# Optimization experiments

Hardware: AMD Instinct MI355X
Metric: run time of the kernel (lower is better)

Reference implementation:

```python
import jax, jax.numpy as jnp
import numpy as np

N = 100000
E = 3_200_000
H = 64
R = 2
NEG = 0.01   # leaky_relu default slope
EPS = 1e-5   # BatchNorm eps


def leaky(x):
    return jnp.where(x > 0, x, NEG * x)


def bn(x, g, b, m, v):
    # BatchNorm1d in eval mode (running statistics)
    return (x - m) * jax.lax.rsqrt(v + EPS) * g + b


def setup_inputs() -> dict:
    key = jax.random.key(0)
    ks = jax.random.split(key, 16)
    d = {}
    d["des"] = jax.random.normal(ks[0], (N, 768), jnp.float32)
    d["num"] = jax.random.normal(ks[1], (N, 5), jnp.float32)
    d["cat"] = jax.random.normal(ks[2], (N, 6), jnp.float32)
    d["edge_index"] = jax.random.randint(ks[3], (2, E), 0, N)
    d["edge_type"] = jax.random.randint(ks[4], (E,), 0, R)

    def lin(k, o, i):
        return (jax.random.normal(k, (o, i), jnp.float32) / np.float32(np.sqrt(i)))

    # projection heads: Linear + BatchNorm1d params
    d["des_W"] = lin(ks[5], H, 768); d["des_b"] = jnp.zeros((H,), jnp.float32)
    d["num_W"] = lin(ks[6], H, 5);   d["num_b"] = jnp.zeros((H,), jnp.float32)
    d["cat_W"] = lin(ks[7], H, 6);   d["cat_b"] = jnp.zeros((H,), jnp.float32)
    for name, kk in (("des", ks[8]), ("num", ks[9]), ("cat", ks[10])):
        d[name + "_g"] = jnp.ones((H,), jnp.float32)
        d[name + "_beta"] = jnp.zeros((H,), jnp.float32)
        d[name + "_m"] = 0.1 * jax.random.normal(kk, (H,), jnp.float32)
        d[name + "_v"] = jnp.ones((H,), jnp.float32)
    # RGCN relation weights [R, in, out] (used as F.linear(x, W[r]) -> x @ W[r].T)
    d["rgcn_W"] = jax.random.normal(ks[11], (R, H, H), jnp.float32) / np.float32(np.sqrt(H))
    # classifier
    d["cls_W1"] = lin(ks[12], H // 2, H); d["cls_b1"] = jnp.zeros((H // 2,), jnp.float32)
    d["cls_W2"] = lin(ks[13], 2, H // 2); d["cls_b2"] = jnp.zeros((2,), jnp.float32)
    return d


def reference(des, num, cat, edge_index, edge_type,
              des_W, des_b, des_g, des_beta, des_m, des_v,
              num_W, num_b, num_g, num_beta, num_m, num_v,
              cat_W, cat_b, cat_g, cat_beta, cat_m, cat_v,
              rgcn_W, cls_W1, cls_b1, cls_W2, cls_b2):
    # feature fusion: three Linear+BN+LeakyReLU branches summed
    x = leaky(bn(des @ des_W.T + des_b, des_g, des_beta, des_m, des_v))
    x = x + leaky(bn(num @ num_W.T + num_b, num_g, num_beta, num_m, num_v))
    x = x + leaky(bn(cat @ cat_W.T + cat_b, cat_g, cat_beta, cat_m, cat_v))

    # SimpleRGCNConv: per-relation linear transform + masked scatter-mean over edges
    src, dst = edge_index[0], edge_index[1]  # PyG: row=source, col=target
    n = x.shape[0]
    acc = jnp.zeros((n, H), x.dtype)
    for r in range(R):
        x_r = x @ rgcn_W[r].T                       # F.linear(x, weight[r])
        mask = (edge_type == r).astype(x.dtype)     # [E]
        msg = x_r[src] * mask[:, None]              # gather + mask
        s = jax.ops.segment_sum(msg, dst, num_segments=n)
        cnt = jax.ops.segment_sum(mask, dst, num_segments=n)
        acc = acc + s / jnp.maximum(cnt, 1.0)[:, None]  # mean; 0 for isolated nodes
    x = leaky(acc / R)  # mean over relations

    # dropout in eval mode is identity; classifier
    h = leaky(x @ cls_W1.T + cls_b1)
    return h @ cls_W2.T + cls_b2
```

## Files before the change

kernel.cpp:

```cpp
#include <hip/hip_runtime.h>

typedef unsigned int u32;
typedef unsigned short u16;

#define NEG 0.01f
#define BN_EPS 1e-5f

typedef __attribute__((ext_vector_type(8))) short bf16x8;
typedef __attribute__((ext_vector_type(4))) float f32x4;

__device__ __forceinline__ float bl(u32 u){ union { u32 i; float f; } c; c.i = u << 16; return c.f; }
__device__ __forceinline__ float bh(u32 u){ union { u32 i; float f; } c; c.i = u & 0xFFFF0000u; return c.f; }
__device__ __forceinline__ u16 f2b(float f){
  union { float f; u32 i; } c; c.f = f;
  u32 t = c.i + 0x7FFFu + ((c.i >> 16) & 1u);
  return (u16)(t >> 16);
}
__device__ __forceinline__ float leaky(float v){ return v > 0.f ? v : NEG * v; }

__global__ __launch_bounds__(256) void k_hist_prep(
    const int* __restrict__ ei, const int* __restrict__ et, int E, int HB, int PB,
    int* __restrict__ deg2,
    const float* __restrict__ desWf, const float* __restrict__ rgcnW,
    const float* __restrict__ W1, u16* __restrict__ tab,
    const float* __restrict__ des, u16* __restrict__ des16, int n)
{
  int bid = blockIdx.x;
  if (bid < HB) {
    int e = bid * 256 + threadIdx.x;
    if (e < E) atomicAdd(&deg2[ei[E + e] * 2 + et[e]], 1);
  } else if (bid < HB + PB) {
    int i = (bid - HB) * 256 + threadIdx.x;
    if (i < 49152) {
      int j = i & 7, lane = (i >> 3) & 63, t = (i >> 9) & 3, k = i >> 11;
      int row = 16 * t + (lane & 15);
      int col = 32 * k + 8 * (lane >> 4) + j;
      tab[i] = f2b(desWf[row * 768 + col]);
    } else if (i < 57344) {
      int j = i - 49152;
      int h = j >> 7, k = j & 127;
      tab[i] = f2b(rgcnW[(k >= 64 ? 4096 : 0) + h * 64 + (k & 63)]);
    } else if (i < 59392) {
      tab[i] = f2b(W1[i - 57344]);
    }
  } else {
    int fb = bid - HB - PB;
    const int tid = threadIdx.x;
    u16* outb = des16 + (size_t)fb * 49152;
    #pragma unroll 4
    for (int it = 0; it < 24; ++it) {
      int s = it * 256 + tid;
      int lane = s & 63;
      int k = (s >> 6) % 24;
      int w = s / 1536;
      int row = fb * 64 + 16 * w + (lane & 15);
      if (row > n - 1) row = n - 1;
      int col = 32 * k + 8 * (lane >> 4);
      const float* p = des + (size_t)row * 768 + col;
      float4 u = *(const float4*)p;
      float4 v = *(const float4*)(p + 4);
      int4 o4;
      o4.x = (int)((u32)f2b(u.x) | ((u32)f2b(u.y) << 16));
      o4.y = (int)((u32)f2b(u.z) | ((u32)f2b(u.w) << 16));
      o4.z = (int)((u32)f2b(v.x) | ((u32)f2b(v.y) << 16));
      o4.w = (int)((u32)f2b(v.z) | ((u32)f2b(v.w) << 16));
      *(int4*)(outb + (size_t)s * 8) = o4;
    }
  }
}

__global__ __launch_bounds__(256) void k_fuse_scan(
    const u16* __restrict__ des16, const float* __restrict__ nump, const float* __restrict__ catp,
    const u16* __restrict__ Wpk, const float* __restrict__ desB,
    const float* __restrict__ numW, const float* __restrict__ numB,
    const float* __restrict__ catW, const float* __restrict__ catB,
    const float* __restrict__ dg, const float* __restrict__ dbe, const float* __restrict__ dm, const float* __restrict__ dv,
    const float* __restrict__ ng, const float* __restrict__ nbe, const float* __restrict__ nm, const float* __restrict__ nv,
    const float* __restrict__ cg, const float* __restrict__ cbe, const float* __restrict__ cm, const float* __restrict__ cv,
    u16* __restrict__ x16, int n,
    const int* __restrict__ deg2, int* __restrict__ offs2, int M)
{
  const int tid  = threadIdx.x;
  const int lane = tid & 63;
  const int w    = tid >> 6;

  if (blockIdx.x == 0) {
    __shared__ int wsum[4];
    __shared__ int carry;
    if (tid == 0) carry = 0;
    __syncthreads();
    for (int base = 0; base < M; base += 1024) {
      int idx = base + tid * 4;
      int4 v = {0, 0, 0, 0};
      if (idx < M) v = *(const int4*)(deg2 + idx);
      int s4 = v.x + v.y + v.z + v.w;
      int s = s4;
      #pragma unroll
      for (int o = 1; o < 64; o <<= 1) { int t = __shfl_up(s, o); if (lane >= o) s += t; }
      if (lane == 63) wsum[w] = s;
      __syncthreads();
      if (tid == 0) {
        int a = wsum[0];
        a += wsum[1]; wsum[1] = a;
        a += wsum[2]; wsum[2] = a;
        a += wsum[3]; wsum[3] = a;
      }
      __syncthreads();
      int wbase = (w == 0) ? 0 : wsum[w - 1];
      int ebase = carry + wbase + (s - s4);
      if (idx < M) {
        int4 o4;
        o4.x = ebase;
        o4.y = ebase + v.x;
        o4.z = ebase + v.x + v.y;
        o4.w = ebase + v.x + v.y + v.z;
        *(int4*)(offs2 + idx) = o4;
      }
      __syncthreads();
      if (tid == 0) carry += wsum[3];
      __syncthreads();
    }
    if (tid == 0) offs2[M] = carry;
    return;
  }

  __shared__ float ync[64][66];

  const int quad = lane >> 4;
  const int l15  = lane & 15;
  const int fb   = blockIdx.x - 1;
  const int rowbase = fb * 64 + 16 * w;

  {
    float nw[5], cw[6];
    #pragma unroll
    for (int j = 0; j < 5; ++j) nw[j] = numW[lane * 5 + j];
    #pragma unroll
    for (int j = 0; j < 6; ++j) cw[j] = catW[lane * 6 + j];
    float An = ng[lane] * rsqrtf(nv[lane] + BN_EPS);
    float Bn = (numB[lane] - nm[lane]) * An + nbe[lane];
    float Ac = cg[lane] * rsqrtf(cv[lane] + BN_EPS);
    float Bc = (catB[lane] - cm[lane]) * Ac + cbe[lane];
    for (int m = 0; m < 16; ++m) {
      int node = rowbase + m; if (node > n - 1) node = n - 1;
      float yn = 0.f, yc = 0.f;
      #pragma unroll
      for (int j = 0; j < 5; ++j) yn = fmaf(nump[node * 5 + j], nw[j], yn);
      #pragma unroll
      for (int j = 0; j < 6; ++j) yc = fmaf(catp[node * 6 + j], cw[j], yc);
      ync[16 * w + m][lane] = leaky(yn * An + Bn) + leaky(yc * Ac + Bc);
    }
  }

  float Ad4[4], Bd4[4];
  #pragma unroll
  for (int t = 0; t < 4; ++t) {
    int nn = 16 * t + l15;
    float A = dg[nn] * rsqrtf(dv[nn] + BN_EPS);
    Ad4[t] = A;
    Bd4[t] = (desB[nn] - dm[nn]) * A + dbe[nn];
  }
  __syncthreads();

  const u16* aP = des16 + (size_t)(fb * 4 + w) * 12288 + lane * 8;
  const u16* bP = Wpk + lane * 8;

  f32x4 acc[4];
  #pragma unroll
  for (int t = 0; t < 4; ++t) acc[t] = (f32x4){0.f, 0.f, 0.f, 0.f};

  #pragma unroll 4
  for (int k = 0; k < 24; ++k) {
    bf16x8 a = *(const bf16x8*)(aP + k * 512);
    acc[0] = __builtin_amdgcn_mfma_f32_16x16x32_bf16(a, *(const bf16x8*)(bP + k * 2048       ), acc[0], 0, 0, 0);
    acc[1] = __builtin_amdgcn_mfma_f32_16x16x32_bf16(a, *(const bf16x8*)(bP + k * 2048 +  512), acc[1], 0, 0, 0);
    acc[2] = __builtin_amdgcn_mfma_f32_16x16x32_bf16(a, *(const bf16x8*)(bP + k * 2048 + 1024), acc[2], 0, 0, 0);
    acc[3] = __builtin_amdgcn_mfma_f32_16x16x32_bf16(a, *(const bf16x8*)(bP + k * 2048 + 1536), acc[3], 0, 0, 0);
  }

  #pragma unroll
  for (int t = 0; t < 4; ++t) {
    #pragma unroll
    for (int r = 0; r < 4; ++r) {
      int m = quad * 4 + r;
      int node = rowbase + m;
      if (node < n) {
        int nn = 16 * t + l15;
        float v = leaky(acc[t][r] * Ad4[t] + Bd4[t]) + ync[16 * w + m][nn];
        x16[(size_t)node * 64 + nn] = f2b(v);
      }
    }
  }
}

__global__ void k_place(const int* __restrict__ ei, const int* __restrict__ et, int E,
                        const int* __restrict__ offs2, int* __restrict__ cur2, int* __restrict__ packed)
{
  int e = blockIdx.x * 256 + threadIdx.x;
  if (e < E) {
    int bin = ei[E + e] * 2 + et[e];
    int pos = offs2[bin] + atomicAdd(&cur2[bin], 1);
    packed[pos] = ei[e];
  }
}

__global__ __launch_bounds__(256) void k_agg(
    const u16* __restrict__ x16, const int* __restrict__ offs2, const int* __restrict__ packed,
    u32* __restrict__ agg, int n)
{
  const int tid = threadIdx.x, lane = tid & 63, w = tid >> 6;
  const int c = lane & 31, half = lane >> 5;

  for (int nd = blockIdx.x * 4 + w; nd < n; nd += gridDim.x * 4) {
    int o0 = offs2[nd * 2], o1 = offs2[nd * 2 + 1], o2 = offs2[nd * 2 + 2];
    float aE[2], aO[2];

    #pragma unroll
    for (int rel = 0; rel < 2; ++rel) {
      int beg = rel ? o1 : o0;
      int end = rel ? o2 : o1;
      float accE = 0.f, accO = 0.f;
      for (int j0 = beg; j0 < end; j0 += 64) {
        int idx = j0 + lane;
        int p = (idx < end) ? packed[idx] : 0;
        p = (p < 0) ? 0 : ((p > n - 1) ? (n - 1) : p);
        int cn = end - j0; if (cn > 64) cn = 64;
        int t = 0;
        for (; t + 16 <= cn; t += 16) {
          int s0 = __shfl(p, t      + half);
          int s1 = __shfl(p, t + 2  + half);
          int s2 = __shfl(p, t + 4  + half);
          int s3 = __shfl(p, t + 6  + half);
          int s4 = __shfl(p, t + 8  + half);
          int s5 = __shfl(p, t + 10 + half);
          int s6 = __shfl(p, t + 12 + half);
          int s7 = __shfl(p, t + 14 + half);
          u32 v0 = *(const u32*)(x16 + (size_t)s0 * 64 + 2 * c);
          u32 v1 = *(const u32*)(x16 + (size_t)s1 * 64 + 2 * c);
          u32 v2 = *(const u32*)(x16 + (size_t)s2 * 64 + 2 * c);
          u32 v3 = *(const u32*)(x16 + (size_t)s3 * 64 + 2 * c);
          u32 v4 = *(const u32*)(x16 + (size_t)s4 * 64 + 2 * c);
          u32 v5 = *(const u32*)(x16 + (size_t)s5 * 64 + 2 * c);
          u32 v6 = *(const u32*)(x16 + (size_t)s6 * 64 + 2 * c);
          u32 v7 = *(const u32*)(x16 + (size_t)s7 * 64 + 2 * c);
          accE += ((bl(v0) + bl(v1)) + (bl(v2) + bl(v3))) + ((bl(v4) + bl(v5)) + (bl(v6) + bl(v7)));
          accO += ((bh(v0) + bh(v1)) + (bh(v2) + bh(v3))) + ((bh(v4) + bh(v5)) + (bh(v6) + bh(v7)));
        }
        for (; t + 8 <= cn; t += 8) {
          int s0 = __shfl(p, t     + half);
          int s1 = __shfl(p, t + 2 + half);
          int s2 = __shfl(p, t + 4 + half);
          int s3 = __shfl(p, t + 6 + half);
          u32 v0 = *(const u32*)(x16 + (size_t)s0 * 64 + 2 * c);
          u32 v1 = *(const u32*)(x16 + (size_t)s1 * 64 + 2 * c);
          u32 v2 = *(const u32*)(x16 + (size_t)s2 * 64 + 2 * c);
          u32 v3 = *(const u32*)(x16 + (size_t)s3 * 64 + 2 * c);
          accE += (bl(v0) + bl(v1)) + (bl(v2) + bl(v3));
          accO += (bh(v0) + bh(v1)) + (bh(v2) + bh(v3));
        }
        for (; t + 2 <= cn; t += 2) {
          int s0 = __shfl(p, t + half);
          u32 v0 = *(const u32*)(x16 + (size_t)s0 * 64 + 2 * c);
          accE += bl(v0); accO += bh(v0);
        }
        if (t < cn) {
          int s0 = __shfl(p, t);
          if (half == 0) {
            u32 v0 = *(const u32*)(x16 + (size_t)s0 * 64 + 2 * c);
            accE += bl(v0); accO += bh(v0);
          }
        }
      }
      accE += __shfl_xor(accE, 32);
      accO += __shfl_xor(accO, 32);
      int cnt = end - beg;
      float sc = 1.f / (float)(cnt > 1 ? cnt : 1);
      aE[rel] = accE * sc;
      aO[rel] = accO * sc;
    }

    float sE = half ? aE[1] : aE[0];
    float sO = half ? aO[1] : aO[0];
    agg[(size_t)nd * 64 + lane] = (u32)f2b(sE) | ((u32)f2b(sO) << 16);
  }
}

__global__ __launch_bounds__(256) void k_mlp(
    const u32* __restrict__ agg, const u16* __restrict__ Wmlp, const u16* __restrict__ W1p,
    const float* __restrict__ b1, const float* __restrict__ W2, const float* __restrict__ b2,
    float2* __restrict__ out, int n)
{
  __shared__ __align__(16) u16 h1[4][16][72];
  __shared__ float h2[4][16][34];

  const int tid = threadIdx.x, lane = tid & 63, w = tid >> 6;
  const int quad = lane >> 4, l15 = lane & 15;
  const int rowbase = blockIdx.x * 64 + 16 * w;

  int rowA = rowbase + l15; if (rowA > n - 1) rowA = n - 1;
  const u16* aRow = (const u16*)(agg + (size_t)rowA * 64);

  f32x4 acc[4];
  #pragma unroll
  for (int t = 0; t < 4; ++t) acc[t] = (f32x4){0.f, 0.f, 0.f, 0.f};
  #pragma unroll
  for (int ks = 0; ks < 4; ++ks) {
    bf16x8 a = *(const bf16x8*)(aRow + ks * 32 + quad * 8);
    #pragma unroll
    for (int t = 0; t < 4; ++t) {
      bf16x8 b = *(const bf16x8*)(Wmlp + (size_t)(16 * t + l15) * 128 + ks * 32 + quad * 8);
      acc[t] = __builtin_amdgcn_mfma_f32_16x16x32_bf16(a, b, acc[t], 0, 0, 0);
    }
  }
  #pragma unroll
  for (int t = 0; t < 4; ++t)
    #pragma unroll
    for (int r = 0; r < 4; ++r) {
      int m = quad * 4 + r;
      h1[w][m][16 * t + l15] = f2b(leaky(0.5f * acc[t][r]));
    }
  __syncthreads();

  f32x4 acc2[2];
  acc2[0] = (f32x4){0.f, 0.f, 0.f, 0.f};
  acc2[1] = (f32x4){0.f, 0.f, 0.f, 0.f};
  #pragma unroll
  for (int ks = 0; ks < 2; ++ks) {
    bf16x8 a = *(const bf16x8*)(&h1[w][l15][ks * 32 + quad * 8]);
    #pragma unroll
    for (int t = 0; t < 2; ++t) {
      bf16x8 b = *(const bf16x8*)(W1p + (size_t)(16 * t + l15) * 64 + ks * 32 + quad * 8);
      acc2[t] = __builtin_amdgcn_mfma_f32_16x16x32_bf16(a, b, acc2[t], 0, 0, 0);
    }
  }
  #pragma unroll
  for (int t = 0; t < 2; ++t)
    #pragma unroll
    for (int r = 0; r < 4; ++r) {
      int m = quad * 4 + r;
      int j = 16 * t + l15;
      h2[w][m][j] = leaky(acc2[t][r] + b1[j]);
    }
  __syncthreads();

  float t0 = 0.f, t1 = 0.f;
  #pragma unroll
  for (int jj = 0; jj < 8; ++jj) {
    int j = quad * 8 + jj;
    float hv = h2[w][l15][j];
    t0 = fmaf(hv, W2[j], t0);
    t1 = fmaf(hv, W2[32 + j], t1);
  }
  t0 += __shfl_xor(t0, 16); t0 += __shfl_xor(t0, 32);
  t1 += __shfl_xor(t1, 16); t1 += __shfl_xor(t1, 32);
  int node = rowbase + l15;
  if (quad == 0 && node < n) {
    float2 q; q.x = t0 + b2[0]; q.y = t1 + b2[1];
    out[node] = q;
  }
}

extern "C" void kernel_launch(void* const* d_in, const int* in_sizes, int n_in,
                              void* d_out, int out_size, void* d_ws, size_t ws_size,
                              hipStream_t stream)
{
  const float* des  = (const float*)d_in[0];
  const float* nump = (const float*)d_in[1];
  const float* catp = (const float*)d_in[2];
  const int* ei   = (const int*)d_in[3];
  const int* et   = (const int*)d_in[4];
  const float* desW = (const float*)d_in[5];
  const float* desB = (const float*)d_in[6];
  const float* numW = (const float*)d_in[7];
  const float* numB = (const float*)d_in[8];
  const float* catW = (const float*)d_in[9];
  const float* catB = (const float*)d_in[10];
  const float* dg  = (const float*)d_in[11];
  const float* dbe = (const float*)d_in[12];
  const float* dm  = (const float*)d_in[13];
  const float* dv  = (const float*)d_in[14];
  const float* ng  = (const float*)d_in[15];
  const float* nbe = (const float*)d_in[16];
  const float* nm  = (const float*)d_in[17];
  const float* nv  = (const float*)d_in[18];
  const float* cg  = (const float*)d_in[19];
  const float* cbe = (const float*)d_in[20];
  const float* cm  = (const float*)d_in[21];
  const float* cv  = (const float*)d_in[22];
  const float* rgcnW = (const float*)d_in[23];
  const float* W1 = (const float*)d_in[24];
  const float* b1 = (const float*)d_in[25];
  const float* W2 = (const float*)d_in[26];
  const float* b2 = (const float*)d_in[27];

  const int N = in_sizes[1] / 5;
  const int E = in_sizes[4];
  const int M = 2 * N;
  const int NB = (N + 63) / 64;

  char* ws = (char*)d_ws;
  u16* tab    = (u16*)ws;                  size_t off = (size_t)59392 * 2;
  off = (off + 255) & ~(size_t)255;
  u16* x16    = (u16*)(ws + off);          off += (size_t)N * 64 * 2;
  u32* agg    = (u32*)(ws + off);          off += (size_t)N * 64 * 4;
  int* deg2   = (int*)(ws + off);          off += (size_t)M * 4;
  int* cur2   = (int*)(ws + off);          off += (size_t)M * 4;
  int* offs2  = (int*)(ws + off);          off += (size_t)(M + 1) * 4;
  off = (off + 255) & ~(size_t)255;
  int* packed = (int*)(ws + off);          off += (size_t)E * 4;
  off = (off + 255) & ~(size_t)255;
  u16* des16  = (u16*)(ws + off);

  u16* Wpk    = tab;
  u16* Wmlp   = tab + 49152;
  u16* W1p    = tab + 57344;

  hipMemsetAsync(deg2, 0, (size_t)M * 8, stream);

  const int HB = (E + 255) / 256;
  const int PB = (59392 + 255) / 256;
  k_hist_prep<<<HB + PB + NB, 256, 0, stream>>>(ei, et, E, HB, PB, deg2,
                                                desW, rgcnW, W1, tab,
                                                des, des16, N);

  k_fuse_scan<<<NB + 1, 256, 0, stream>>>(des16, nump, catp, Wpk, desB, numW, numB, catW, catB,
                                          dg, dbe, dm, dv, ng, nbe, nm, nv, cg, cbe, cm, cv,
                                          x16, N, deg2, offs2, M);

  k_place<<<(E + 255) / 256, 256, 0, stream>>>(ei, et, E, offs2, cur2, packed);
  k_agg<<<2048, 256, 0, stream>>>(x16, offs2, packed, agg, N);
  k_mlp<<<(N + 63) / 64, 256, 0, stream>>>(agg, Wmlp, W1p, b1, W2, b2, (float2*)d_out, N);
}
```

Baseline: 1.063 ms.

## Pad histogram counters to 64-byte stride, split hist kernel, coalesce des conversion

```diff
diff --git a/kernel.cpp b/kernel.cpp
--- a/kernel.cpp
+++ b/kernel.cpp
@@ -18,19 +18,26 @@
 }
 __device__ __forceinline__ float leaky(float v){ return v > 0.f ? v : NEG * v; }
 
-__global__ __launch_bounds__(256) void k_hist_prep(
-    const int* __restrict__ ei, const int* __restrict__ et, int E, int HB, int PB,
-    int* __restrict__ deg2,
+__global__ __launch_bounds__(256) void k_hist(
+    const int* __restrict__ ei, const int* __restrict__ et, int E,
+    int* __restrict__ deg2p)
+{
+  int e = blockIdx.x * 256 + threadIdx.x;
+  if (e < E) {
+    int bin = ei[E + e] * 2 + et[e];
+    atomicAdd(&deg2p[(size_t)bin << 4], 1);
+  }
+}
+
+__global__ __launch_bounds__(256) void k_prep_conv(
+    int PB,
     const float* __restrict__ desWf, const float* __restrict__ rgcnW,
     const float* __restrict__ W1, u16* __restrict__ tab,
     const float* __restrict__ des, u16* __restrict__ des16, int n)
 {
   int bid = blockIdx.x;
-  if (bid < HB) {
-    int e = bid * 256 + threadIdx.x;
-    if (e < E) atomicAdd(&deg2[ei[E + e] * 2 + et[e]], 1);
-  } else if (bid < HB + PB) {
-    int i = (bid - HB) * 256 + threadIdx.x;
+  if (bid < PB) {
+    int i = bid * 256 + threadIdx.x;
     if (i < 49152) {
       int j = i & 7, lane = (i >> 3) & 63, t = (i >> 9) & 3, k = i >> 11;
       int row = 16 * t + (lane & 15);
@@ -44,19 +51,17 @@
       tab[i] = f2b(W1[i - 57344]);
     }
   } else {
-    int fb = bid - HB - PB;
+    int fb = bid - PB;
     const int tid = threadIdx.x;
     u16* outb = des16 + (size_t)fb * 49152;
     #pragma unroll 4
     for (int it = 0; it < 24; ++it) {
-      int s = it * 256 + tid;
-      int lane = s & 63;
-      int k = (s >> 6) % 24;
-      int w = s / 1536;
-      int row = fb * 64 + 16 * w + (lane & 15);
+      int g = it * 256 + tid;
+      int r      = g / 96;
+      int colblk = g - r * 96;
+      int row = fb * 64 + r;
       if (row > n - 1) row = n - 1;
-      int col = 32 * k + 8 * (lane >> 4);
-      const float* p = des + (size_t)row * 768 + col;
+      const float* p = des + (size_t)row * 768 + colblk * 8;
       float4 u = *(const float4*)p;
       float4 v = *(const float4*)(p + 4);
       int4 o4;
@@ -64,6 +69,9 @@
       o4.y = (int)((u32)f2b(u.z) | ((u32)f2b(u.w) << 16));
       o4.z = (int)((u32)f2b(v.x) | ((u32)f2b(v.y) << 16));
       o4.w = (int)((u32)f2b(v.z) | ((u32)f2b(v.w) << 16));
+      int w  = r >> 4, l15 = r & 15;
+      int k  = colblk >> 2, q = colblk & 3;
+      int s  = (w * 24 + k) * 64 + q * 16 + l15;
       *(int4*)(outb + (size_t)s * 8) = o4;
     }
   }
@@ -78,7 +86,7 @@
     const float* __restrict__ ng, const float* __restrict__ nbe, const float* __restrict__ nm, const float* __restrict__ nv,
     const float* __restrict__ cg, const float* __restrict__ cbe, const float* __restrict__ cm, const float* __restrict__ cv,
     u16* __restrict__ x16, int n,
-    const int* __restrict__ deg2, int* __restrict__ offs2, int M)
+    const int* __restrict__ deg2p, int* __restrict__ offs2, int M)
 {
   const int tid  = threadIdx.x;
   const int lane = tid & 63;
@@ -92,7 +100,12 @@
     for (int base = 0; base < M; base += 1024) {
       int idx = base + tid * 4;
       int4 v = {0, 0, 0, 0};
-      if (idx < M) v = *(const int4*)(deg2 + idx);
+      if (idx < M) {
+        v.x = deg2p[(size_t)(idx + 0) << 4];
+        v.y = deg2p[(size_t)(idx + 1) << 4];
+        v.z = deg2p[(size_t)(idx + 2) << 4];
+        v.w = deg2p[(size_t)(idx + 3) << 4];
+      }
       int s4 = v.x + v.y + v.z + v.w;
       int s = s4;
       #pragma unroll
@@ -194,12 +207,12 @@
 }
 
 __global__ void k_place(const int* __restrict__ ei, const int* __restrict__ et, int E,
-                        const int* __restrict__ offs2, int* __restrict__ cur2, int* __restrict__ packed)
+                        const int* __restrict__ offs2, int* __restrict__ cur2p, int* __restrict__ packed)
 {
   int e = blockIdx.x * 256 + threadIdx.x;
   if (e < E) {
     int bin = ei[E + e] * 2 + et[e];
-    int pos = offs2[bin] + atomicAdd(&cur2[bin], 1);
+    int pos = offs2[bin] + atomicAdd(&cur2p[(size_t)bin << 4], 1);
     packed[pos] = ei[e];
   }
 }
@@ -403,8 +416,8 @@
   off = (off + 255) & ~(size_t)255;
   u16* x16    = (u16*)(ws + off);          off += (size_t)N * 64 * 2;
   u32* agg    = (u32*)(ws + off);          off += (size_t)N * 64 * 4;
-  int* deg2   = (int*)(ws + off);          off += (size_t)M * 4;
-  int* cur2   = (int*)(ws + off);          off += (size_t)M * 4;
+  int* deg2p  = (int*)(ws + off);          off += (size_t)M * 64;
+  int* cur2p  = (int*)(ws + off);          off += (size_t)M * 64;
   int* offs2  = (int*)(ws + off);          off += (size_t)(M + 1) * 4;
   off = (off + 255) & ~(size_t)255;
   int* packed = (int*)(ws + off);          off += (size_t)E * 4;
@@ -415,19 +428,19 @@
   u16* Wmlp   = tab + 49152;
   u16* W1p    = tab + 57344;
 
-  hipMemsetAsync(deg2, 0, (size_t)M * 8, stream);
+  hipMemsetAsync(deg2p, 0, (size_t)M * 128, stream);
 
   const int HB = (E + 255) / 256;
   const int PB = (59392 + 255) / 256;
-  k_hist_prep<<<HB + PB + NB, 256, 0, stream>>>(ei, et, E, HB, PB, deg2,
-                                                desW, rgcnW, W1, tab,
-                                                des, des16, N);
+
+  k_hist<<<HB, 256, 0, stream>>>(ei, et, E, deg2p);
+  k_prep_conv<<<PB + NB, 256, 0, stream>>>(PB, desW, rgcnW, W1, tab, des, des16, N);
 
   k_fuse_scan<<<NB + 1, 256, 0, stream>>>(des16, nump, catp, Wpk, desB, numW, numB, catW, catB,
                                           dg, dbe, dm, dv, ng, nbe, nm, nv, cg, cbe, cm, cv,
-                                          x16, N, deg2, offs2, M);
-
-  k_place<<<(E + 255) / 256, 256, 0, stream>>>(ei, et, E, offs2, cur2, packed);
+                                          x16, N, deg2p, offs2, M);
+
+  k_place<<<(E + 255) / 256, 256, 0, stream>>>(ei, et, E, offs2, cur2p, packed);
   k_agg<<<2048, 256, 0, stream>>>(x16, offs2, packed, agg, N);
   k_mlp<<<(N + 63) / 64, 256, 0, stream>>>(agg, Wmlp, W1p, b1, W2, b2, (float2*)d_out, N);
 }
```

New measurement: 1.341 ms. 1.26x slower.
